# Performance work log

Hardware: AMD Instinct MI355X
Metric: run time of the kernel (lower is better)

Reference implementation:

```python
import jax, jax.numpy as jnp
import numpy as np

B, H, W = 8, 64, 64
DIM_RGB, DIM_PL, EMBED, OUT = 256, 256, 128, 256
BN_EPS = 1e-5


def conv1x1(x, w, b=None):
    # x: (B,C,H,W), w: (D,C) -> (B,D,H,W)
    y = jnp.einsum('bchw,dc->bdhw', x, w)
    if b is not None:
        y = y + b[None, :, None, None]
    return y


def spatial_attention(q, k, v, scale):
    # q,k,v: (B,D,H,W)
    b, d, h, w = q.shape
    n = h * w
    qf = q.reshape(b, d, n).transpose(0, 2, 1)   # (B,N,D)
    kf = k.reshape(b, d, n)                       # (B,D,N)
    vf = v.reshape(b, d, n).transpose(0, 2, 1)   # (B,N,D)
    attn = jax.nn.softmax(jnp.einsum('bnd,bdm->bnm', qf, kf) * scale, axis=-1)
    out = jnp.einsum('bnm,bmd->bnd', attn, vf)   # (B,N,D)
    return out.transpose(0, 2, 1).reshape(b, d, h, w)


def setup_inputs() -> dict:
    key = jax.random.key(0)
    ks = jax.random.split(key, 20)
    s = 0.05
    inp = {
        'f_rgb': jax.random.normal(ks[0], (B, DIM_RGB, H, W), jnp.float32),
        'f_pl': jax.random.normal(ks[1], (B, DIM_PL, H, W), jnp.float32),
        'w_q_rgb': jax.random.normal(ks[2], (EMBED, DIM_RGB), jnp.float32) * s,
        'b_q_rgb': jax.random.normal(ks[3], (EMBED,), jnp.float32) * s,
        'w_k_pl': jax.random.normal(ks[4], (EMBED, DIM_PL), jnp.float32) * s,
        'b_k_pl': jax.random.normal(ks[5], (EMBED,), jnp.float32) * s,
        'w_v_pl': jax.random.normal(ks[6], (EMBED, DIM_PL), jnp.float32) * s,
        'b_v_pl': jax.random.normal(ks[7], (EMBED,), jnp.float32) * s,
        'w_q_pl': jax.random.normal(ks[8], (EMBED, DIM_PL), jnp.float32) * s,
        'b_q_pl': jax.random.normal(ks[9], (EMBED,), jnp.float32) * s,
        'w_k_rgb': jax.random.normal(ks[10], (EMBED, DIM_RGB), jnp.float32) * s,
        'b_k_rgb': jax.random.normal(ks[11], (EMBED,), jnp.float32) * s,
        'w_v_rgb': jax.random.normal(ks[12], (EMBED, DIM_RGB), jnp.float32) * s,
        'b_v_rgb': jax.random.normal(ks[13], (EMBED,), jnp.float32) * s,
        'w_proj': jax.random.normal(ks[14], (OUT, 2 * EMBED), jnp.float32) * s,
        'bn_gamma': jnp.ones((OUT,), jnp.float32),
        'bn_beta': jnp.zeros((OUT,), jnp.float32),
        'bn_mean': jax.random.normal(ks[15], (OUT,), jnp.float32) * 0.01,
        'bn_var': jax.random.uniform(ks[16], (OUT,), jnp.float32, 0.5, 1.5),
    }
    return inp


def reference(f_rgb, f_pl, w_q_rgb, b_q_rgb, w_k_pl, b_k_pl, w_v_pl, b_v_pl,
              w_q_pl, b_q_pl, w_k_rgb, b_k_rgb, w_v_rgb, b_v_rgb,
              w_proj, bn_gamma, bn_beta, bn_mean, bn_var):
    scale = EMBED ** -0.5
    out_rgb2pl = spatial_attention(
        conv1x1(f_rgb, w_q_rgb, b_q_rgb),
        conv1x1(f_pl, w_k_pl, b_k_pl),
        conv1x1(f_pl, w_v_pl, b_v_pl), scale)
    out_pl2rgb = spatial_attention(
        conv1x1(f_pl, w_q_pl, b_q_pl),
        conv1x1(f_rgb, w_k_rgb, b_k_rgb),
        conv1x1(f_rgb, w_v_rgb, b_v_rgb), scale)
    combined = jnp.concatenate([out_rgb2pl, out_pl2rgb], axis=1)  # (B,2E,H,W)
    y = conv1x1(combined, w_proj)  # no bias
    # BatchNorm2d (inference form) + ReLU
    inv = bn_gamma * jax.lax.rsqrt(bn_var + BN_EPS)
    y = y * inv[None, :, None, None] + (bn_beta - bn_mean * inv)[None, :, None, None]
    return jax.nn.relu(y)
```

## Files before the change

kernel.cpp:

```cpp
#include <hip/hip_runtime.h>
#include <hip/hip_bf16.h>
#include <hip/hip_fp16.h>

typedef _Float16 f16;
typedef _Float16 f16x8 __attribute__((ext_vector_type(8)));
typedef _Float16 f16x4 __attribute__((ext_vector_type(4)));
typedef float f32x4 __attribute__((ext_vector_type(4)));

#define NP   4096
#define NB   8
#define CINC 256
#define EMB  128
#define OUTC 256
#define BN_EPS 1e-5f

__device__ __forceinline__ bool bf16_mode(const unsigned int* det) {
    return *det == 0x3F803F80u;
}

template<bool BF>
__device__ __forceinline__ float ldf(const void* p, size_t i) {
    if (BF) return __bfloat162float(((const __hip_bfloat16*)p)[i]);
    return ((const float*)p)[i];
}

template<bool BF>
__global__ __launch_bounds__(256) void proj3_kernel(
    const void* __restrict__ X,
    const void* __restrict__ W0, const void* __restrict__ B0,
    const void* __restrict__ W1, const void* __restrict__ B1,
    const void* __restrict__ W2, const void* __restrict__ B2,
    f16* __restrict__ outQ, f16* __restrict__ outK, f16* __restrict__ outV,
    const unsigned int* __restrict__ det)
{
    if (BF != bf16_mode(det)) return;
    const int m0 = blockIdx.x * 128;
    const int t  = blockIdx.y;
    const int b  = blockIdx.z;
    const int tid = threadIdx.x;
    const int w = tid >> 6, lane = tid & 63, quad = lane >> 4, lr = lane & 15;

    const void* W  = (t == 0) ? W0 : (t == 1) ? W1 : W2;
    const void* Bi = (t == 0) ? B0 : (t == 1) ? B1 : B2;

    __shared__ __align__(16) f16 smem[128 * 72 * 2];
    f16* Al = smem;
    f16* Bl = smem + 128 * 72;

    f32x4 acc[2][8];
    #pragma unroll
    for (int mi = 0; mi < 2; ++mi)
        #pragma unroll
        for (int ni = 0; ni < 8; ++ni) acc[mi][ni] = (f32x4){0.f, 0.f, 0.f, 0.f};

    for (int kt = 0; kt < 4; ++kt) {
        const int kc0 = kt * 64;
        __syncthreads();
        for (int s = tid; s < 1024; s += 256) {
            const int n = s & 127, cg = s >> 7;
            f16 tmp[8];
            #pragma unroll
            for (int j = 0; j < 8; ++j)
                tmp[j] = (f16)ldf<BF>(X, ((size_t)b * CINC + kc0 + cg * 8 + j) * NP + m0 + n);
            *(f16x8*)&Al[n * 72 + cg * 8] = *(const f16x8*)tmp;
        }
        for (int s = tid; s < 1024; s += 256) {
            const int d = s >> 3, cg = s & 7;
            f16 tmp[8];
            #pragma unroll
            for (int j = 0; j < 8; ++j)
                tmp[j] = (f16)ldf<BF>(W, (size_t)d * CINC + kc0 + cg * 8 + j);
            *(f16x8*)&Bl[d * 72 + cg * 8] = *(const f16x8*)tmp;
        }
        __syncthreads();
        #pragma unroll
        for (int ks = 0; ks < 2; ++ks) {
            f16x8 af[2], bfr[8];
            #pragma unroll
            for (int mi = 0; mi < 2; ++mi)
                af[mi] = *(const f16x8*)&Al[(w * 32 + mi * 16 + lr) * 72 + ks * 32 + quad * 8];
            #pragma unroll
            for (int ni = 0; ni < 8; ++ni)
                bfr[ni] = *(const f16x8*)&Bl[(ni * 16 + lr) * 72 + ks * 32 + quad * 8];
            #pragma unroll
            for (int mi = 0; mi < 2; ++mi)
                #pragma unroll
                for (int ni = 0; ni < 8; ++ni)
                    acc[mi][ni] = __builtin_amdgcn_mfma_f32_16x16x32_f16(
                        af[mi], bfr[ni], acc[mi][ni], 0, 0, 0);
        }
    }

    float bias[8];
    #pragma unroll
    for (int ni = 0; ni < 8; ++ni) bias[ni] = ldf<BF>(Bi, ni * 16 + lr);

    if (t < 2) {
        f16* out = (t == 0) ? outQ : outK;
        #pragma unroll
        for (int mi = 0; mi < 2; ++mi)
            #pragma unroll
            for (int ni = 0; ni < 8; ++ni)
                #pragma unroll
                for (int r = 0; r < 4; ++r) {
                    const int n = m0 + w * 32 + mi * 16 + quad * 4 + r;
                    out[((size_t)b * NP + n) * EMB + ni * 16 + lr] =
                        (f16)(acc[mi][ni][r] + bias[ni]);
                }
    } else {
        __syncthreads();
        f16* T = smem;
        #pragma unroll
        for (int mi = 0; mi < 2; ++mi)
            #pragma unroll
            for (int ni = 0; ni < 8; ++ni)
                #pragma unroll
                for (int r = 0; r < 4; ++r)
                    T[(ni * 16 + lr) * 136 + w * 32 + mi * 16 + quad * 4 + r] =
                        (f16)(acc[mi][ni][r] + bias[ni]);
        __syncthreads();
        for (int s = tid; s < 2048; s += 256) {
            const int d = s >> 4, n8 = (s & 15) * 8;
            *(f16x8*)&outV[((size_t)b * EMB + d) * NP + m0 + n8] =
                *(const f16x8*)&T[d * 136 + n8];
        }
    }
}

__global__ __launch_bounds__(256, 2) void attn_kernel(
    const f16* __restrict__ Qt, const f16* __restrict__ Kt,
    const f16* __restrict__ Vn, f16* __restrict__ combT)
{
    const int dir = blockIdx.z, b = blockIdx.y;
    const int n0 = blockIdx.x * 128;
    const int tid = threadIdx.x;
    const int w = tid >> 6, lane = tid & 63, quad = lane >> 4, lr = lane & 15;

    const f16* Q = Qt + ((size_t)dir * NB + b) * NP * EMB;
    const f16* K = Kt + ((size_t)dir * NB + b) * NP * EMB;
    const f16* V = Vn + ((size_t)dir * NB + b) * EMB * NP;

    __shared__ __align__(16) f16 Kl[64][136];
    __shared__ __align__(16) f16 Vl[128][72];

    const int qbase = n0 + w * 32;

    f16x8 qf[2][4];
    #pragma unroll
    for (int nt = 0; nt < 2; ++nt)
        #pragma unroll
        for (int cc = 0; cc < 4; ++cc) {
            f16x8 q = *(const f16x8*)&Q[(size_t)(qbase + nt * 16 + lr) * EMB + cc * 32 + quad * 8];
            #pragma unroll
            for (int k = 0; k < 8; ++k)
                q[k] = q[k] * (f16)0.12752749f;
            qf[nt][cc] = q;
        }

    f32x4 O[2][8];
    #pragma unroll
    for (int nt = 0; nt < 2; ++nt)
        #pragma unroll
        for (int dt = 0; dt < 8; ++dt) O[nt][dt] = (f32x4){0.f, 0.f, 0.f, 0.f};
    float rs[2] = {0.f, 0.f};

    for (int m0 = 0; m0 < NP; m0 += 64) {
        __syncthreads();
        #pragma unroll
        for (int s = 0; s < 4; ++s) {
            const int i = s * 256 + tid;
            const int mm = i >> 4, dc = i & 15;
            *(f16x8*)&Kl[mm][dc * 8] = *(const f16x8*)&K[(size_t)(m0 + mm) * EMB + dc * 8];
        }
        #pragma unroll
        for (int s = 0; s < 4; ++s) {
            const int i = s * 256 + tid;
            const int d = i >> 3, mc = i & 7;
            *(f16x8*)&Vl[d][mc * 8] = *(const f16x8*)&V[(size_t)d * NP + m0 + mc * 8];
        }
        __syncthreads();

        #pragma unroll
        for (int ms = 0; ms < 4; ++ms) {
            f16x8 kf[4];
            #pragma unroll
            for (int cc = 0; cc < 4; ++cc)
                kf[cc] = *(const f16x8*)&Kl[ms * 16 + lr][cc * 32 + quad * 8];

            f16x4 ppk[2];
            #pragma unroll
            for (int nt = 0; nt < 2; ++nt) {
                f32x4 s = (f32x4){0.f, 0.f, 0.f, 0.f};
                #pragma unroll
                for (int cc = 0; cc < 4; ++cc)
                    s = __builtin_amdgcn_mfma_f32_16x16x32_f16(kf[cc], qf[nt][cc], s, 0, 0, 0);
                float e0 = __builtin_amdgcn_exp2f(s[0]);
                float e1 = __builtin_amdgcn_exp2f(s[1]);
                float e2 = __builtin_amdgcn_exp2f(s[2]);
                float e3 = __builtin_amdgcn_exp2f(s[3]);
                rs[nt] += (e0 + e1) + (e2 + e3);
                f16x4 pp;
                pp[0] = (f16)e0; pp[1] = (f16)e1; pp[2] = (f16)e2; pp[3] = (f16)e3;
                ppk[nt] = pp;
            }

            #pragma unroll
            for (int dt = 0; dt < 8; ++dt) {
                const f16x4 vf = *(const f16x4*)&Vl[dt * 16 + lr][ms * 16 + quad * 4];
                #pragma unroll
                for (int nt = 0; nt < 2; ++nt)
                    O[nt][dt] = __builtin_amdgcn_mfma_f32_16x16x16f16(
                        ppk[nt], vf, O[nt][dt], 0, 0, 0);
            }
        }
    }

    #pragma unroll
    for (int nt = 0; nt < 2; ++nt) {
        rs[nt] += __shfl_xor(rs[nt], 16);
        rs[nt] += __shfl_xor(rs[nt], 32);
    }
    #pragma unroll
    for (int nt = 0; nt < 2; ++nt) {
        float iv[4];
        #pragma unroll
        for (int r = 0; r < 4; ++r)
            iv[r] = 1.0f / __shfl(rs[nt], quad * 4 + r, 64);
        #pragma unroll
        for (int dt = 0; dt < 8; ++dt)
            #pragma unroll
            for (int r = 0; r < 4; ++r) {
                const int n = qbase + nt * 16 + quad * 4 + r;
                combT[((size_t)b * NP + n) * OUTC + dir * EMB + dt * 16 + lr] =
                    (f16)(O[nt][dt][r] * iv[r]);
            }
    }
}

template<bool BF>
__global__ __launch_bounds__(256) void proj_out_kernel(
    const f16* __restrict__ combT, const void* __restrict__ Wp,
    const void* __restrict__ G, const void* __restrict__ Be,
    const void* __restrict__ Mu, const void* __restrict__ Va,
    void* __restrict__ out, const unsigned int* __restrict__ det)
{
    if (BF != bf16_mode(det)) return;
    const int m0 = blockIdx.x * 128;
    const int o0 = blockIdx.y * 128;
    const int b  = blockIdx.z;
    const int tid = threadIdx.x;
    const int w = tid >> 6, lane = tid & 63, quad = lane >> 4, lr = lane & 15;

    __shared__ __align__(16) f16 smem[128 * 72 * 2];
    f16* Al = smem;
    f16* Bl = smem + 128 * 72;

    f32x4 acc[2][8];
    #pragma unroll
    for (int mi = 0; mi < 2; ++mi)
        #pragma unroll
        for (int ni = 0; ni < 8; ++ni) acc[mi][ni] = (f32x4){0.f, 0.f, 0.f, 0.f};

    for (int kt = 0; kt < 4; ++kt) {
        const int kc0 = kt * 64;
        __syncthreads();
        for (int s = tid; s < 1024; s += 256) {
            const int n = s >> 3, cg = s & 7;
            *(f16x8*)&Al[n * 72 + cg * 8] =
                *(const f16x8*)&combT[((size_t)b * NP + m0 + n) * OUTC + kc0 + cg * 8];
        }
        for (int s = tid; s < 1024; s += 256) {
            const int d = s >> 3, cg = s & 7;
            f16 tmp[8];
            #pragma unroll
            for (int j = 0; j < 8; ++j)
                tmp[j] = (f16)ldf<BF>(Wp, (size_t)(o0 + d) * OUTC + kc0 + cg * 8 + j);
            *(f16x8*)&Bl[d * 72 + cg * 8] = *(const f16x8*)tmp;
        }
        __syncthreads();
        #pragma unroll
        for (int ks = 0; ks < 2; ++ks) {
            f16x8 af[2], bfr[8];
            #pragma unroll
            for (int mi = 0; mi < 2; ++mi)
                af[mi] = *(const f16x8*)&Al[(w * 32 + mi * 16 + lr) * 72 + ks * 32 + quad * 8];
            #pragma unroll
            for (int ni = 0; ni < 8; ++ni)
                bfr[ni] = *(const f16x8*)&Bl[(ni * 16 + lr) * 72 + ks * 32 + quad * 8];
            #pragma unroll
            for (int mi = 0; mi < 2; ++mi)
                #pragma unroll
                for (int ni = 0; ni < 8; ++ni)
                    acc[mi][ni] = __builtin_amdgcn_mfma_f32_16x16x32_f16(
                        af[mi], bfr[ni], acc[mi][ni], 0, 0, 0);
        }
    }

    __syncthreads();
    f16* T = smem;
    #pragma unroll
    for (int ni = 0; ni < 8; ++ni) {
        const int o = o0 + ni * 16 + lr;
        const float iv = ldf<BF>(G, o) * rsqrtf(ldf<BF>(Va, o) + BN_EPS);
        const float sh = ldf<BF>(Be, o) - ldf<BF>(Mu, o) * iv;
        #pragma unroll
        for (int mi = 0; mi < 2; ++mi)
            #pragma unroll
            for (int r = 0; r < 4; ++r)
                T[(ni * 16 + lr) * 136 + w * 32 + mi * 16 + quad * 4 + r] =
                    (f16)fmaxf(acc[mi][ni][r] * iv + sh, 0.f);
    }
    __syncthreads();
    for (int s = tid; s < 2048; s += 256) {
        const int o = s >> 4, n8 = (s & 15) * 8;
        const f16x8 v = *(const f16x8*)&T[o * 136 + n8];
        const size_t off = ((size_t)b * OUTC + o0 + o) * NP + m0 + n8;
        if (BF) {
            __hip_bfloat16* ob = (__hip_bfloat16*)out;
            #pragma unroll
            for (int k = 0; k < 8; ++k) ob[off + k] = __float2bfloat16((float)v[k]);
        } else {
            float* of = (float*)out;
            #pragma unroll
            for (int k = 0; k < 8; ++k) of[off + k] = (float)v[k];
        }
    }
}

extern "C" void kernel_launch(void* const* d_in, const int* in_sizes, int n_in,
                              void* d_out, int out_size, void* d_ws, size_t ws_size,
                              hipStream_t stream) {
    const void* f_rgb   = d_in[0];
    const void* f_pl    = d_in[1];
    const void* w_q_rgb = d_in[2];  const void* b_q_rgb = d_in[3];
    const void* w_k_pl  = d_in[4];  const void* b_k_pl  = d_in[5];
    const void* w_v_pl  = d_in[6];  const void* b_v_pl  = d_in[7];
    const void* w_q_pl  = d_in[8];  const void* b_q_pl  = d_in[9];
    const void* w_k_rgb = d_in[10]; const void* b_k_rgb = d_in[11];
    const void* w_v_rgb = d_in[12]; const void* b_v_rgb = d_in[13];
    const void* w_proj  = d_in[14];
    const unsigned int* det = (const unsigned int*)d_in[15];
    const void* bn_g = d_in[15]; const void* bn_b = d_in[16];
    const void* bn_m = d_in[17]; const void* bn_v = d_in[18];

    const size_t TSZ = (size_t)2 * NB * NP * EMB;
    const size_t DSZ = (size_t)NB * NP * EMB;
    f16* Qt    = (f16*)d_ws;
    f16* Kt    = Qt + TSZ;
    f16* Vn    = Kt + TSZ;
    f16* combT = Vn + TSZ;

    dim3 gp(32, 3, 8);
    proj3_kernel<false><<<gp, 256, 0, stream>>>(f_rgb, w_q_rgb, b_q_rgb, w_k_rgb, b_k_rgb,
        w_v_rgb, b_v_rgb, Qt + 0 * DSZ, Kt + 1 * DSZ, Vn + 1 * DSZ, det);
    proj3_kernel<true ><<<gp, 256, 0, stream>>>(f_rgb, w_q_rgb, b_q_rgb, w_k_rgb, b_k_rgb,
        w_v_rgb, b_v_rgb, Qt + 0 * DSZ, Kt + 1 * DSZ, Vn + 1 * DSZ, det);
    proj3_kernel<false><<<gp, 256, 0, stream>>>(f_pl, w_q_pl, b_q_pl, w_k_pl, b_k_pl,
        w_v_pl, b_v_pl, Qt + 1 * DSZ, Kt + 0 * DSZ, Vn + 0 * DSZ, det);
    proj3_kernel<true ><<<gp, 256, 0, stream>>>(f_pl, w_q_pl, b_q_pl, w_k_pl, b_k_pl,
        w_v_pl, b_v_pl, Qt + 1 * DSZ, Kt + 0 * DSZ, Vn + 0 * DSZ, det);

    attn_kernel<<<dim3(32, 8, 2), 256, 0, stream>>>(Qt, Kt, Vn, combT);

    dim3 go(32, 2, 8);
    proj_out_kernel<false><<<go, 256, 0, stream>>>(combT, w_proj, bn_g, bn_b, bn_m, bn_v,
                                                   d_out, det);
    proj_out_kernel<true ><<<go, 256, 0, stream>>>(combT, w_proj, bn_g, bn_b, bn_m, bn_v,
                                                   d_out, det);
}
```

Before: 389.3 us.

## Pre-convert inputs to fp16, stream K from registers, drop bf16 dispatch

```diff
diff --git a/kernel.cpp b/kernel.cpp
--- a/kernel.cpp
+++ b/kernel.cpp
@@ -14,34 +14,71 @@
 #define OUTC 256
 #define BN_EPS 1e-5f
 
-__device__ __forceinline__ bool bf16_mode(const unsigned int* det) {
-    return *det == 0x3F803F80u;
-}
-
-template<bool BF>
-__device__ __forceinline__ float ldf(const void* p, size_t i) {
-    if (BF) return __bfloat162float(((const __hip_bfloat16*)p)[i]);
-    return ((const float*)p)[i];
-}
-
-template<bool BF>
-__global__ __launch_bounds__(256) void proj3_kernel(
-    const void* __restrict__ X,
-    const void* __restrict__ W0, const void* __restrict__ B0,
-    const void* __restrict__ W1, const void* __restrict__ B1,
-    const void* __restrict__ W2, const void* __restrict__ B2,
-    f16* __restrict__ outQ, f16* __restrict__ outK, f16* __restrict__ outV,
-    const unsigned int* __restrict__ det)
-{
-    if (BF != bf16_mode(det)) return;
+#define DSZ  ((size_t)NB * NP * EMB)
+#define TSZ  (2 * DSZ)
+
+__global__ __launch_bounds__(256) void prep_x_kernel(
+    const float* __restrict__ X, f16* __restrict__ XT)
+{
+    const int n0 = blockIdx.x * 64, c0 = blockIdx.y * 64, b = blockIdx.z;
+    const int tid = threadIdx.x;
+    __shared__ __align__(16) f16 Xl[64][72];
+    const int nl = tid & 63, cq = tid >> 6;
+    #pragma unroll
+    for (int cc = 0; cc < 16; ++cc) {
+        const int c = c0 + cc * 4 + cq;
+        Xl[nl][cc * 4 + cq] = (f16)X[((size_t)b * CINC + c) * NP + n0 + nl];
+    }
+    __syncthreads();
+    #pragma unroll
+    for (int i = 0; i < 2; ++i) {
+        const int s2 = i * 256 + tid;
+        const int n = s2 >> 3, cg = s2 & 7;
+        *(f16x8*)&XT[((size_t)b * NP + n0 + n) * CINC + c0 + cg * 8] =
+            *(const f16x8*)&Xl[n][cg * 8];
+    }
+}
+
+__global__ __launch_bounds__(256) void prep_w_kernel(
+    const float* __restrict__ w0, const float* __restrict__ w1,
+    const float* __restrict__ w2, const float* __restrict__ w3,
+    const float* __restrict__ w4, const float* __restrict__ w5,
+    const float* __restrict__ wp,
+    const float* __restrict__ b0, const float* __restrict__ b1,
+    const float* __restrict__ b2, const float* __restrict__ b3,
+    const float* __restrict__ b4, const float* __restrict__ b5,
+    f16* __restrict__ Wf, f16* __restrict__ Bf)
+{
+    const int idx = blockIdx.x * 256 + threadIdx.x;
+    if (idx < 196608) {
+        const int p = idx >> 15, off = idx & 32767;
+        const float* w = p == 0 ? w0 : p == 1 ? w1 : p == 2 ? w2
+                       : p == 3 ? w3 : p == 4 ? w4 : w5;
+        Wf[idx] = (f16)w[off];
+    } else if (idx < 262144) {
+        Wf[idx] = (f16)wp[idx - 196608];
+    } else if (idx < 262912) {
+        const int r = idx - 262144, p = r >> 7, off = r & 127;
+        const float* bb = p == 0 ? b0 : p == 1 ? b1 : p == 2 ? b2
+                        : p == 3 ? b3 : p == 4 ? b4 : b5;
+        Bf[r] = (f16)bb[off];
+    }
+}
+
+__global__ __launch_bounds__(256) void proj6_kernel(
+    const f16* __restrict__ XT, const f16* __restrict__ Wf,
+    const f16* __restrict__ Bf, const int pbase,
+    f16* __restrict__ Qt, f16* __restrict__ Kt, f16* __restrict__ Vn)
+{
     const int m0 = blockIdx.x * 128;
-    const int t  = blockIdx.y;
+    const int p  = pbase + blockIdx.y;
     const int b  = blockIdx.z;
+    const int s  = (p >= 3) ? 1 : 0;
+    const int j  = p - s * 3;
     const int tid = threadIdx.x;
     const int w = tid >> 6, lane = tid & 63, quad = lane >> 4, lr = lane & 15;
 
-    const void* W  = (t == 0) ? W0 : (t == 1) ? W1 : W2;
-    const void* Bi = (t == 0) ? B0 : (t == 1) ? B1 : B2;
+    const f16* W = Wf + (size_t)p * 32768;
 
     __shared__ __align__(16) f16 smem[128 * 72 * 2];
     f16* Al = smem;
@@ -56,21 +93,19 @@
     for (int kt = 0; kt < 4; ++kt) {
         const int kc0 = kt * 64;
         __syncthreads();
-        for (int s = tid; s < 1024; s += 256) {
-            const int n = s & 127, cg = s >> 7;
-            f16 tmp[8];
-            #pragma unroll
-            for (int j = 0; j < 8; ++j)
-                tmp[j] = (f16)ldf<BF>(X, ((size_t)b * CINC + kc0 + cg * 8 + j) * NP + m0 + n);
-            *(f16x8*)&Al[n * 72 + cg * 8] = *(const f16x8*)tmp;
-        }
-        for (int s = tid; s < 1024; s += 256) {
-            const int d = s >> 3, cg = s & 7;
-            f16 tmp[8];
-            #pragma unroll
-            for (int j = 0; j < 8; ++j)
-                tmp[j] = (f16)ldf<BF>(W, (size_t)d * CINC + kc0 + cg * 8 + j);
-            *(f16x8*)&Bl[d * 72 + cg * 8] = *(const f16x8*)tmp;
+        #pragma unroll
+        for (int i = 0; i < 4; ++i) {
+            const int s2 = i * 256 + tid;
+            const int n = s2 >> 3, cg = s2 & 7;
+            *(f16x8*)&Al[n * 72 + cg * 8] =
+                *(const f16x8*)&XT[((size_t)b * NP + m0 + n) * CINC + kc0 + cg * 8];
+        }
+        #pragma unroll
+        for (int i = 0; i < 4; ++i) {
+            const int s2 = i * 256 + tid;
+            const int d = s2 >> 3, cg = s2 & 7;
+            *(f16x8*)&Bl[d * 72 + cg * 8] =
+                *(const f16x8*)&W[(size_t)d * CINC + kc0 + cg * 8];
         }
         __syncthreads();
         #pragma unroll
@@ -93,10 +128,10 @@
 
     float bias[8];
     #pragma unroll
-    for (int ni = 0; ni < 8; ++ni) bias[ni] = ldf<BF>(Bi, ni * 16 + lr);
-
-    if (t < 2) {
-        f16* out = (t == 0) ? outQ : outK;
+    for (int ni = 0; ni < 8; ++ni) bias[ni] = (float)Bf[p * 128 + ni * 16 + lr];
+
+    if (j < 2) {
+        f16* out = (j == 0) ? (Qt + (size_t)s * DSZ) : (Kt + (size_t)(1 - s) * DSZ);
         #pragma unroll
         for (int mi = 0; mi < 2; ++mi)
             #pragma unroll
@@ -108,6 +143,7 @@
                         (f16)(acc[mi][ni][r] + bias[ni]);
                 }
     } else {
+        f16* outV = Vn + (size_t)(1 - s) * DSZ;
         __syncthreads();
         f16* T = smem;
         #pragma unroll
@@ -119,8 +155,8 @@
                     T[(ni * 16 + lr) * 136 + w * 32 + mi * 16 + quad * 4 + r] =
                         (f16)(acc[mi][ni][r] + bias[ni]);
         __syncthreads();
-        for (int s = tid; s < 2048; s += 256) {
-            const int d = s >> 4, n8 = (s & 15) * 8;
+        for (int s2 = tid; s2 < 2048; s2 += 256) {
+            const int d = s2 >> 4, n8 = (s2 & 15) * 8;
             *(f16x8*)&outV[((size_t)b * EMB + d) * NP + m0 + n8] =
                 *(const f16x8*)&T[d * 136 + n8];
         }
@@ -131,16 +167,16 @@
     const f16* __restrict__ Qt, const f16* __restrict__ Kt,
     const f16* __restrict__ Vn, f16* __restrict__ combT)
 {
-    const int dir = blockIdx.z, b = blockIdx.y;
-    const int n0 = blockIdx.x * 128;
+    const int bid = blockIdx.x;
+    const int g = bid & 15, dir = g >> 3, b = g & 7;
+    const int n0 = (bid >> 4) * 128;
     const int tid = threadIdx.x;
     const int w = tid >> 6, lane = tid & 63, quad = lane >> 4, lr = lane & 15;
 
     const f16* Q = Qt + ((size_t)dir * NB + b) * NP * EMB;
     const f16* K = Kt + ((size_t)dir * NB + b) * NP * EMB;
-    const f16* V = Vn + ((size_t)dir * NB + b) * EMB * NP;
-
-    __shared__ __align__(16) f16 Kl[64][136];
+    const f16* V = Vn + ((size_t)dir * NB + b) * (size_t)EMB * NP;
+
     __shared__ __align__(16) f16 Vl[128][72];
 
     const int qbase = n0 + w * 32;
@@ -164,53 +200,55 @@
         for (int dt = 0; dt < 8; ++dt) O[nt][dt] = (f32x4){0.f, 0.f, 0.f, 0.f};
     float rs[2] = {0.f, 0.f};
 
+    f16x8 kfp[4];
+    #pragma unroll
+    for (int cc = 0; cc < 4; ++cc)
+        kfp[cc] = *(const f16x8*)&K[(size_t)lr * EMB + cc * 32 + quad * 8];
+
     for (int m0 = 0; m0 < NP; m0 += 64) {
         __syncthreads();
         #pragma unroll
-        for (int s = 0; s < 4; ++s) {
-            const int i = s * 256 + tid;
-            const int mm = i >> 4, dc = i & 15;
-            *(f16x8*)&Kl[mm][dc * 8] = *(const f16x8*)&K[(size_t)(m0 + mm) * EMB + dc * 8];
-        }
-        #pragma unroll
-        for (int s = 0; s < 4; ++s) {
-            const int i = s * 256 + tid;
-            const int d = i >> 3, mc = i & 7;
+        for (int i = 0; i < 4; ++i) {
+            const int s2 = i * 256 + tid;
+            const int d = s2 >> 3, mc = s2 & 7;
             *(f16x8*)&Vl[d][mc * 8] = *(const f16x8*)&V[(size_t)d * NP + m0 + mc * 8];
         }
         __syncthreads();
 
         #pragma unroll
         for (int ms = 0; ms < 4; ++ms) {
-            f16x8 kf[4];
-            #pragma unroll
-            for (int cc = 0; cc < 4; ++cc)
-                kf[cc] = *(const f16x8*)&Kl[ms * 16 + lr][cc * 32 + quad * 8];
-
+            f32x4 sa[2];
+            sa[0] = (f32x4){0.f, 0.f, 0.f, 0.f};
+            sa[1] = (f32x4){0.f, 0.f, 0.f, 0.f};
+            #pragma unroll
+            for (int cc = 0; cc < 4; ++cc) {
+                sa[0] = __builtin_amdgcn_mfma_f32_16x16x32_f16(kfp[cc], qf[0][cc], sa[0], 0, 0, 0);
+                sa[1] = __builtin_amdgcn_mfma_f32_16x16x32_f16(kfp[cc], qf[1][cc], sa[1], 0, 0, 0);
+            }
+            {
+                const int nm0 = (ms == 3) ? ((m0 + 64) & (NP - 1)) : m0;
+                const int nms = (ms + 1) & 3;
+                #pragma unroll
+                for (int cc = 0; cc < 4; ++cc)
+                    kfp[cc] = *(const f16x8*)&K[(size_t)(nm0 + nms * 16 + lr) * EMB + cc * 32 + quad * 8];
+            }
             f16x4 ppk[2];
             #pragma unroll
             for (int nt = 0; nt < 2; ++nt) {
-                f32x4 s = (f32x4){0.f, 0.f, 0.f, 0.f};
-                #pragma unroll
-                for (int cc = 0; cc < 4; ++cc)
-                    s = __builtin_amdgcn_mfma_f32_16x16x32_f16(kf[cc], qf[nt][cc], s, 0, 0, 0);
-                float e0 = __builtin_amdgcn_exp2f(s[0]);
-                float e1 = __builtin_amdgcn_exp2f(s[1]);
-                float e2 = __builtin_amdgcn_exp2f(s[2]);
-                float e3 = __builtin_amdgcn_exp2f(s[3]);
+                const float e0 = __builtin_amdgcn_exp2f(sa[nt][0]);
+                const float e1 = __builtin_amdgcn_exp2f(sa[nt][1]);
+                const float e2 = __builtin_amdgcn_exp2f(sa[nt][2]);
+                const float e3 = __builtin_amdgcn_exp2f(sa[nt][3]);
                 rs[nt] += (e0 + e1) + (e2 + e3);
                 f16x4 pp;
                 pp[0] = (f16)e0; pp[1] = (f16)e1; pp[2] = (f16)e2; pp[3] = (f16)e3;
                 ppk[nt] = pp;
             }
-
             #pragma unroll
             for (int dt = 0; dt < 8; ++dt) {
                 const f16x4 vf = *(const f16x4*)&Vl[dt * 16 + lr][ms * 16 + quad * 4];
-                #pragma unroll
-                for (int nt = 0; nt < 2; ++nt)
-                    O[nt][dt] = __builtin_amdgcn_mfma_f32_16x16x16f16(
-                        ppk[nt], vf, O[nt][dt], 0, 0, 0);
+                O[0][dt] = __builtin_amdgcn_mfma_f32_16x16x16f16(ppk[0], vf, O[0][dt], 0, 0, 0);
+                O[1][dt] = __builtin_amdgcn_mfma_f32_16x16x16f16(ppk[1], vf, O[1][dt], 0, 0, 0);
             }
         }
     }
@@ -237,14 +275,12 @@
     }
 }
 
-template<bool BF>
 __global__ __launch_bounds__(256) void proj_out_kernel(
-    const f16* __restrict__ combT, const void* __restrict__ Wp,
-    const void* __restrict__ G, const void* __restrict__ Be,
-    const void* __restrict__ Mu, const void* __restrict__ Va,
-    void* __restrict__ out, const unsigned int* __restrict__ det)
-{
-    if (BF != bf16_mode(det)) return;
+    const f16* __restrict__ combT, const f16* __restrict__ Wp,
+    const float* __restrict__ G, const float* __restrict__ Be,
+    const float* __restrict__ Mu, const float* __restrict__ Va,
+    float* __restrict__ out)
+{
     const int m0 = blockIdx.x * 128;
     const int o0 = blockIdx.y * 128;
     const int b  = blockIdx.z;
@@ -264,18 +300,19 @@
     for (int kt = 0; kt < 4; ++kt) {
         const int kc0 = kt * 64;
         __syncthreads();
-        for (int s = tid; s < 1024; s += 256) {
-            const int n = s >> 3, cg = s & 7;
+        #pragma unroll
+        for (int i = 0; i < 4; ++i) {
+            const int s2 = i * 256 + tid;
+            const int n = s2 >> 3, cg = s2 & 7;
             *(f16x8*)&Al[n * 72 + cg * 8] =
                 *(const f16x8*)&combT[((size_t)b * NP + m0 + n) * OUTC + kc0 + cg * 8];
         }
-        for (int s = tid; s < 1024; s += 256) {
-            const int d = s >> 3, cg = s & 7;
-            f16 tmp[8];
-            #pragma unroll
-            for (int j = 0; j < 8; ++j)
-                tmp[j] = (f16)ldf<BF>(Wp, (size_t)(o0 + d) * OUTC + kc0 + cg * 8 + j);
-            *(f16x8*)&Bl[d * 72 + cg * 8] = *(const f16x8*)tmp;
+        #pragma unroll
+        for (int i = 0; i < 4; ++i) {
+            const int s2 = i * 256 + tid;
+            const int d = s2 >> 3, cg = s2 & 7;
+            *(f16x8*)&Bl[d * 72 + cg * 8] =
+                *(const f16x8*)&Wp[(size_t)(o0 + d) * OUTC + kc0 + cg * 8];
         }
         __syncthreads();
         #pragma unroll
@@ -301,8 +338,8 @@
     #pragma unroll
     for (int ni = 0; ni < 8; ++ni) {
         const int o = o0 + ni * 16 + lr;
-        const float iv = ldf<BF>(G, o) * rsqrtf(ldf<BF>(Va, o) + BN_EPS);
-        const float sh = ldf<BF>(Be, o) - ldf<BF>(Mu, o) * iv;
+        const float iv = G[o] * rsqrtf(Va[o] + BN_EPS);
+        const float sh = Be[o] - Mu[o] * iv;
         #pragma unroll
         for (int mi = 0; mi < 2; ++mi)
             #pragma unroll
@@ -311,60 +348,49 @@
                     (f16)fmaxf(acc[mi][ni][r] * iv + sh, 0.f);
     }
     __syncthreads();
-    for (int s = tid; s < 2048; s += 256) {
-        const int o = s >> 4, n8 = (s & 15) * 8;
+    for (int s2 = tid; s2 < 2048; s2 += 256) {
+        const int o = s2 >> 4, n8 = (s2 & 15) * 8;
         const f16x8 v = *(const f16x8*)&T[o * 136 + n8];
         const size_t off = ((size_t)b * OUTC + o0 + o) * NP + m0 + n8;
-        if (BF) {
-            __hip_bfloat16* ob = (__hip_bfloat16*)out;
-            #pragma unroll
-            for (int k = 0; k < 8; ++k) ob[off + k] = __float2bfloat16((float)v[k]);
-        } else {
-            float* of = (float*)out;
-            #pragma unroll
-            for (int k = 0; k < 8; ++k) of[off + k] = (float)v[k];
-        }
+        #pragma unroll
+        for (int k = 0; k < 8; ++k) out[off + k] = (float)v[k];
     }
 }
 
 extern "C" void kernel_launch(void* const* d_in, const int* in_sizes, int n_in,
                               void* d_out, int out_size, void* d_ws, size_t ws_size,
                               hipStream_t stream) {
-    const void* f_rgb   = d_in[0];
-    const void* f_pl    = d_in[1];
-    const void* w_q_rgb = d_in[2];  const void* b_q_rgb = d_in[3];
-    const void* w_k_pl  = d_in[4];  const void* b_k_pl  = d_in[5];
-    const void* w_v_pl  = d_in[6];  const void* b_v_pl  = d_in[7];
-    const void* w_q_pl  = d_in[8];  const void* b_q_pl  = d_in[9];
-    const void* w_k_rgb = d_in[10]; const void* b_k_rgb = d_in[11];
-    const void* w_v_rgb = d_in[12]; const void* b_v_rgb = d_in[13];
-    const void* w_proj  = d_in[14];
-    const unsigned int* det = (const unsigned int*)d_in[15];
-    const void* bn_g = d_in[15]; const void* bn_b = d_in[16];
-    const void* bn_m = d_in[17]; const void* bn_v = d_in[18];
-
-    const size_t TSZ = (size_t)2 * NB * NP * EMB;
-    const size_t DSZ = (size_t)NB * NP * EMB;
-    f16* Qt    = (f16*)d_ws;
-    f16* Kt    = Qt + TSZ;
-    f16* Vn    = Kt + TSZ;
-    f16* combT = Vn + TSZ;
-
-    dim3 gp(32, 3, 8);
-    proj3_kernel<false><<<gp, 256, 0, stream>>>(f_rgb, w_q_rgb, b_q_rgb, w_k_rgb, b_k_rgb,
-        w_v_rgb, b_v_rgb, Qt + 0 * DSZ, Kt + 1 * DSZ, Vn + 1 * DSZ, det);
-    proj3_kernel<true ><<<gp, 256, 0, stream>>>(f_rgb, w_q_rgb, b_q_rgb, w_k_rgb, b_k_rgb,
-        w_v_rgb, b_v_rgb, Qt + 0 * DSZ, Kt + 1 * DSZ, Vn + 1 * DSZ, det);
-    proj3_kernel<false><<<gp, 256, 0, stream>>>(f_pl, w_q_pl, b_q_pl, w_k_pl, b_k_pl,
-        w_v_pl, b_v_pl, Qt + 1 * DSZ, Kt + 0 * DSZ, Vn + 0 * DSZ, det);
-    proj3_kernel<true ><<<gp, 256, 0, stream>>>(f_pl, w_q_pl, b_q_pl, w_k_pl, b_k_pl,
-        w_v_pl, b_v_pl, Qt + 1 * DSZ, Kt + 0 * DSZ, Vn + 0 * DSZ, det);
-
-    attn_kernel<<<dim3(32, 8, 2), 256, 0, stream>>>(Qt, Kt, Vn, combT);
-
-    dim3 go(32, 2, 8);
-    proj_out_kernel<false><<<go, 256, 0, stream>>>(combT, w_proj, bn_g, bn_b, bn_m, bn_v,
-                                                   d_out, det);
-    proj_out_kernel<true ><<<go, 256, 0, stream>>>(combT, w_proj, bn_g, bn_b, bn_m, bn_v,
-                                                   d_out, det);
-}
+    const float* f_rgb   = (const float*)d_in[0];
+    const float* f_pl    = (const float*)d_in[1];
+    const float* w_q_rgb = (const float*)d_in[2];  const float* b_q_rgb = (const float*)d_in[3];
+    const float* w_k_pl  = (const float*)d_in[4];  const float* b_k_pl  = (const float*)d_in[5];
+    const float* w_v_pl  = (const float*)d_in[6];  const float* b_v_pl  = (const float*)d_in[7];
+    const float* w_q_pl  = (const float*)d_in[8];  const float* b_q_pl  = (const float*)d_in[9];
+    const float* w_k_rgb = (const float*)d_in[10]; const float* b_k_rgb = (const float*)d_in[11];
+    const float* w_v_rgb = (const float*)d_in[12]; const float* b_v_rgb = (const float*)d_in[13];
+    const float* w_proj  = (const float*)d_in[14];
+    const float* bn_g    = (const float*)d_in[15]; const float* bn_b = (const float*)d_in[16];
+    const float* bn_m    = (const float*)d_in[17]; const float* bn_v = (const float*)d_in[18];
+
+    f16* Qt = (f16*)d_ws;
+    f16* Kt = Qt + TSZ;
+    f16* Vn = Kt + TSZ;
+    f16* XT = Vn + TSZ;
+    f16* Wf = XT + (size_t)NB * NP * CINC;
+    f16* Bf = Wf + 262144;
+    f16* combT = XT;
+
+    prep_w_kernel<<<1027, 256, 0, stream>>>(
+        w_q_rgb, w_k_rgb, w_v_rgb, w_q_pl, w_k_pl, w_v_pl, w_proj,
+        b_q_rgb, b_k_rgb, b_v_rgb, b_q_pl, b_k_pl, b_v_pl, Wf, Bf);
+
+    prep_x_kernel<<<dim3(64, 4, 8), 256, 0, stream>>>(f_rgb, XT);
+    proj6_kernel<<<dim3(32, 3, 8), 256, 0, stream>>>(XT, Wf, Bf, 0, Qt, Kt, Vn);
+    prep_x_kernel<<<dim3(64, 4, 8), 256, 0, stream>>>(f_pl, XT);
+    proj6_kernel<<<dim3(32, 3, 8), 256, 0, stream>>>(XT, Wf, Bf, 3, Qt, Kt, Vn);
+
+    attn_kernel<<<512, 256, 0, stream>>>(Qt, Kt, Vn, combT);
+
+    proj_out_kernel<<<dim3(32, 2, 8), 256, 0, stream>>>(
+        combT, Wf + 196608, bn_g, bn_b, bn_m, bn_v, (float*)d_out);
+}
```

New measurement: 507.5 us. 1.3x slower.
